# Kernel optimization log

Hardware: AMD Instinct MI355X
Metric: run time of the kernel (lower is better)

## Reference

```python
import jax, jax.numpy as jnp
import numpy as np

B = 16          # frames in batch
N = 16384       # atoms (num_nodes)
R = 1024        # residues (segments)
D = 320         # input_dim
BINS = 32       # adaptive-pool feature bins (output_size_per_segment[1])
H = 512         # mlp_hidden_dim
COND = 3        # conditioner dim (X_ref)
EPS = 1e-5


def setup_inputs() -> dict:
    key = jax.random.key(0)
    ks = jax.random.split(key, 8)
    x = jax.random.normal(ks[0], (B * N, D), dtype=jnp.float32)
    cond = jax.random.normal(ks[1], (N, COND), dtype=jnp.float32)
    # sorted residue ids -> contiguous variable-size segments, like real residues
    seg_ids = jnp.sort(jax.random.randint(ks[2], (N,), 0, R, dtype=jnp.int32))
    W1 = jax.random.normal(ks[3], (BINS + COND, H), dtype=jnp.float32) * 0.05
    b1 = jnp.zeros((H,), jnp.float32)
    gamma = jnp.ones((H,), jnp.float32)
    beta = jnp.zeros((H,), jnp.float32)
    bn_mean = jnp.zeros((H,), jnp.float32)
    bn_var = jnp.ones((H,), jnp.float32)
    W2 = jax.random.normal(ks[4], (H, 3), dtype=jnp.float32) * 0.05
    b2 = jnp.zeros((3,), jnp.float32)
    return {"x": x, "cond": cond, "seg_ids": seg_ids, "W1": W1, "b1": b1,
            "gamma": gamma, "beta": beta, "bn_mean": bn_mean, "bn_var": bn_var,
            "W2": W2, "b2": b2}


def reference(x, cond, seg_ids, W1, b1, gamma, beta, bn_mean, bn_var, W2, b2):
    # x: [B*N, D] atom embeddings
    x3 = x.reshape(B, N, D)
    # --- per-residue AdaptiveAvgPool2d((1, BINS)) as a fused segment mean ---
    # output height 1 == mean over all atoms of the residue
    counts = jax.ops.segment_sum(jnp.ones((N,), x.dtype), seg_ids, num_segments=R)
    sums = jax.vmap(lambda xb: jax.ops.segment_sum(xb, seg_ids, num_segments=R))(x3)  # [B,R,D]
    seg_mean = sums / jnp.maximum(counts, 1.0)[None, :, None]
    # adaptive width D -> BINS (D divisible by BINS => exact chunk means)
    pooled = seg_mean.reshape(B, R, BINS, D // BINS).mean(-1)  # [B,R,BINS]
    # --- broadcast residue feature back to atoms, concat conditioner ---
    per_atom = pooled[:, seg_ids, :]                           # [B,N,BINS]
    cond_b = jnp.broadcast_to(cond[None], (B, N, COND))
    feat = jnp.concatenate([per_atom, cond_b], axis=-1).reshape(B * N, BINS + COND)
    # --- decoder MLP: Linear -> ReLU -> BatchNorm1d(eval) -> Linear ---
    h = jnp.maximum(feat @ W1 + b1, 0.0)
    h = (h - bn_mean) * jax.lax.rsqrt(bn_var + EPS) * gamma + beta
    out = h @ W2 + b2                                          # [B*N, 3]
    return out
```

## Files before the change

kernel.cpp:

```cpp
#include <hip/hip_runtime.h>
#include <math.h>

#define B_ 16
#define N_ 16384
#define R_ 1024
#define D_ 320
#define BINS_ 32
#define H_ 512
#define EPS_ 1e-5f
#define AP 516
#define EP 260

__global__ __launch_bounds__(256) void k_prep(const int* __restrict__ seg,
                      const float* __restrict__ gamma, const float* __restrict__ beta,
                      const float* __restrict__ mean, const float* __restrict__ var,
                      const float* __restrict__ W2, const float* __restrict__ b2,
                      int* __restrict__ off, float* __restrict__ W2f,
                      float* __restrict__ bias3, float* __restrict__ pooled){
  __shared__ float red[3 * 256];
  int blk = blockIdx.x, tid = threadIdx.x;
  if (blk < 5){
    int g = blk * 256 + tid;
    if (g <= R_){
      int lo = 0, hi = N_;
      while (lo < hi){ int mid = (lo + hi) >> 1; if (seg[mid] < g) lo = mid + 1; else hi = mid; }
      off[g] = lo;
    }
  } else if (blk == 5){
    float p0 = 0.f, p1 = 0.f, p2 = 0.f;
    for (int h = tid; h < H_; h += 256){
      float c = gamma[h] / sqrtf(var[h] + EPS_);
      float d = beta[h] - mean[h] * c;
      float w0 = W2[h * 3 + 0], w1 = W2[h * 3 + 1], w2 = W2[h * 3 + 2];
      W2f[h * 3 + 0] = c * w0; W2f[h * 3 + 1] = c * w1; W2f[h * 3 + 2] = c * w2;
      p0 += d * w0; p1 += d * w1; p2 += d * w2;
    }
    red[tid] = p0; red[256 + tid] = p1; red[512 + tid] = p2;
    __syncthreads();
    for (int s = 128; s > 0; s >>= 1){
      if (tid < s){
        red[tid] += red[tid + s];
        red[256 + tid] += red[256 + tid + s];
        red[512 + tid] += red[512 + tid + s];
      }
      __syncthreads();
    }
    if (tid < 3) bias3[tid] = b2[tid] + red[tid * 256];
  } else {
    float4 z = {0.f, 0.f, 0.f, 0.f};
    float4* p4 = (float4*)pooled;
    const int total4 = B_ * R_ * BINS_ / 4;
    for (int i = (blk - 6) * 256 + tid; i < total4; i += 32 * 256) p4[i] = z;
  }
}

__global__ __launch_bounds__(320) void k_pool(const float* __restrict__ x,
                                              const int* __restrict__ seg,
                                              float* __restrict__ pooled){
  __shared__ int sseg[64];
  __shared__ __align__(16) float red2[4 * 320];
  int c = blockIdx.x, b = blockIdx.y, tid = threadIdx.x;
  int base = c * 64;
  if (tid < 64) sseg[tid] = seg[base + tid];
  __syncthreads();
  int rowoff = tid / 80;
  int col4 = tid - rowoff * 80;
  const float4* xp = (const float4*)x + ((size_t)b * N_ + base) * 80 + col4;
  int i = 0;
  while (i < 64){
    int sg = sseg[i];
    int e = i + 1;
    while (e < 64 && sseg[e] == sg) e++;
    float4 acc = {0.f, 0.f, 0.f, 0.f};
    for (int r = i + rowoff; r < e; r += 4){
      float4 v = xp[(size_t)r * 80];
      acc.x += v.x; acc.y += v.y; acc.z += v.z; acc.w += v.w;
    }
    *(float4*)&red2[rowoff * 320 + col4 * 4] = acc;
    __syncthreads();
    if (tid < 32){
      float s = 0.f;
      #pragma unroll
      for (int ro = 0; ro < 4; ro++)
        #pragma unroll
        for (int j = 0; j < 10; j++) s += red2[ro * 320 + tid * 10 + j];
      atomicAdd(&pooled[((size_t)b * R_ + sg) * BINS_ + tid], s);
    }
    __syncthreads();
    i = e;
  }
}

__global__ __launch_bounds__(256) void k_main(const float* __restrict__ pooled, const float* __restrict__ cond,
                      const float* __restrict__ W1, const float* __restrict__ b1,
                      const int* __restrict__ off, const float* __restrict__ W2f,
                      const float* __restrict__ bias3, float* __restrict__ out){
  __shared__ __align__(16) float P[B_ * BINS_];
  __shared__ __align__(16) float A[B_ * AP];
  __shared__ __align__(16) float E[16 * EP];
  __shared__ float condT[16 * 3];
  int tid = threadIdx.x;
  int r = blockIdx.x;
  int s = off[r];
  int cnt = off[r + 1] - s;
  if (cnt == 0) return;

  float sc = 1.0f / (float)(cnt * 10);
  for (int i = tid; i < B_ * BINS_; i += 256)
    P[i] = pooled[(size_t)((i >> 5) * R_ + r) * BINS_ + (i & 31)] * sc;
  __syncthreads();

  for (int h = tid; h < H_; h += 256){
    float bb = b1[h];
    float acc[B_];
    #pragma unroll
    for (int b = 0; b < B_; b++) acc[b] = bb;
    #pragma unroll
    for (int k = 0; k < BINS_; k++){
      float w = W1[k * H_ + h];
      #pragma unroll
      for (int b = 0; b < B_; b++) acc[b] += P[b * BINS_ + k] * w;
    }
    #pragma unroll
    for (int b = 0; b < B_; b++) A[b * AP + h] = acc[b];
  }

  int a = tid >> 4, b = tid & 15;
  for (int t0 = 0; t0 < cnt; t0 += 16){
    int na = min(16, cnt - t0);
    __syncthreads();
    if (tid < 48){
      int aa = tid / 3, cc = tid % 3;
      condT[tid] = (aa < na) ? cond[(size_t)(s + t0 + aa) * 3 + cc] : 0.f;
    }
    __syncthreads();
    float o0 = 0.f, o1 = 0.f, o2 = 0.f;
    int ae = a < na ? a : 0;
    for (int hc = 0; hc < 2; hc++){
      int h = (hc << 8) + tid;
      float w0 = W1[32 * H_ + h], w1 = W1[33 * H_ + h], w2 = W1[34 * H_ + h];
      for (int aa = 0; aa < na; aa++)
        E[aa * EP + tid] = condT[aa * 3] * w0 + condT[aa * 3 + 1] * w1 + condT[aa * 3 + 2] * w2;
      __syncthreads();
      const float* Ap = &A[b * AP + (hc << 8)];
      const float* Ep = &E[ae * EP];
      const float* Wp = &W2f[(hc << 8) * 3];
      #pragma unroll 4
      for (int hp = 0; hp < 256; hp += 4){
        float4 av = *(const float4*)(Ap + hp);
        float4 ev = *(const float4*)(Ep + hp);
        const float* w = Wp + hp * 3;
        float z;
        z = av.x + ev.x; z = fmaxf(z, 0.f); o0 = fmaf(z, w[0], o0); o1 = fmaf(z, w[1], o1); o2 = fmaf(z, w[2], o2);
        z = av.y + ev.y; z = fmaxf(z, 0.f); o0 = fmaf(z, w[3], o0); o1 = fmaf(z, w[4], o1); o2 = fmaf(z, w[5], o2);
        z = av.z + ev.z; z = fmaxf(z, 0.f); o0 = fmaf(z, w[6], o0); o1 = fmaf(z, w[7], o1); o2 = fmaf(z, w[8], o2);
        z = av.w + ev.w; z = fmaxf(z, 0.f); o0 = fmaf(z, w[9], o0); o1 = fmaf(z, w[10], o1); o2 = fmaf(z, w[11], o2);
      }
      __syncthreads();
    }
    if (a < na){
      size_t oi = ((size_t)b * N_ + (size_t)(s + t0 + a)) * 3;
      out[oi + 0] = o0 + bias3[0];
      out[oi + 1] = o1 + bias3[1];
      out[oi + 2] = o2 + bias3[2];
    }
  }
}

extern "C" void kernel_launch(void* const* d_in, const int* in_sizes, int n_in,
                              void* d_out, int out_size, void* d_ws, size_t ws_size,
                              hipStream_t stream) {
  const float* x      = (const float*)d_in[0];
  const float* cond   = (const float*)d_in[1];
  const int*   seg    = (const int*)  d_in[2];
  const float* W1     = (const float*)d_in[3];
  const float* b1     = (const float*)d_in[4];
  const float* gamma  = (const float*)d_in[5];
  const float* beta   = (const float*)d_in[6];
  const float* bnmean = (const float*)d_in[7];
  const float* bnvar  = (const float*)d_in[8];
  const float* W2     = (const float*)d_in[9];
  const float* b2     = (const float*)d_in[10];
  float* out = (float*)d_out;

  char* ws = (char*)d_ws;
  int*   seg_off = (int*)ws;
  float* W2f     = (float*)(ws + 8192);
  float* bias3   = (float*)(ws + 14592);
  float* pooled  = (float*)(ws + 16384);

  k_prep<<<dim3(38), dim3(256), 0, stream>>>(seg, gamma, beta, bnmean, bnvar, W2, b2,
                                             seg_off, W2f, bias3, pooled);
  k_pool<<<dim3(N_ / 64, B_), dim3(320), 0, stream>>>(x, seg, pooled);
  k_main<<<dim3(R_), dim3(256), 0, stream>>>(pooled, cond, W1, b1, seg_off, W2f, bias3, out);
}
```

Before: 638.8 us.

## Make segment pooling wave-local with ballot-based boundaries, no block barriers

The pooling kernel now gives each 64-atom chunk to a single wavefront. Segment boundaries come from a shuffle and ballot, and each lane sums five strided columns across the rows. The per-segment reduction happens in wave-private shared memory, so the two block-wide barriers per segment run are gone. The trade is scalar loads in place of float4 loads, and one wave now serially reads every row of a segment run instead of four threads sharing the rows.

```diff
diff --git a/kernel.cpp b/kernel.cpp
--- a/kernel.cpp
+++ b/kernel.cpp
@@ -54,40 +54,39 @@
   }
 }
 
-__global__ __launch_bounds__(320) void k_pool(const float* __restrict__ x,
+__global__ __launch_bounds__(256) void k_pool(const float* __restrict__ x,
                                               const int* __restrict__ seg,
                                               float* __restrict__ pooled){
-  __shared__ int sseg[64];
-  __shared__ __align__(16) float red2[4 * 320];
-  int c = blockIdx.x, b = blockIdx.y, tid = threadIdx.x;
+  __shared__ __align__(16) float red[4 * 320];
+  int tid = threadIdx.x;
+  int wid = tid >> 6, lane = tid & 63;
+  int c = blockIdx.x * 4 + wid;
+  int b = blockIdx.y;
   int base = c * 64;
-  if (tid < 64) sseg[tid] = seg[base + tid];
-  __syncthreads();
-  int rowoff = tid / 80;
-  int col4 = tid - rowoff * 80;
-  const float4* xp = (const float4*)x + ((size_t)b * N_ + base) * 80 + col4;
-  int i = 0;
-  while (i < 64){
-    int sg = sseg[i];
-    int e = i + 1;
-    while (e < 64 && sseg[e] == sg) e++;
-    float4 acc = {0.f, 0.f, 0.f, 0.f};
-    for (int r = i + rowoff; r < e; r += 4){
-      float4 v = xp[(size_t)r * 80];
-      acc.x += v.x; acc.y += v.y; acc.z += v.z; acc.w += v.w;
+  int my_seg = seg[base + lane];
+  int prev = __shfl_up(my_seg, 1);
+  bool bnd = (lane == 0) || (my_seg != prev);
+  unsigned long long mask = __ballot(bnd);
+  const float* xp = x + ((size_t)b * N_ + base) * D_ + lane;
+  float* wred = &red[wid * 320];
+  while (mask){
+    int i = __builtin_ctzll(mask);
+    mask &= mask - 1;
+    int e = mask ? __builtin_ctzll(mask) : 64;
+    int sg = __shfl(my_seg, i);
+    float a0 = 0.f, a1 = 0.f, a2 = 0.f, a3 = 0.f, a4 = 0.f;
+    const float* rp = xp + (size_t)i * D_;
+    for (int r = i; r < e; r++, rp += D_){
+      a0 += rp[0]; a1 += rp[64]; a2 += rp[128]; a3 += rp[192]; a4 += rp[256];
     }
-    *(float4*)&red2[rowoff * 320 + col4 * 4] = acc;
-    __syncthreads();
-    if (tid < 32){
+    wred[lane] = a0; wred[64 + lane] = a1; wred[128 + lane] = a2;
+    wred[192 + lane] = a3; wred[256 + lane] = a4;
+    if (lane < 32){
       float s = 0.f;
       #pragma unroll
-      for (int ro = 0; ro < 4; ro++)
-        #pragma unroll
-        for (int j = 0; j < 10; j++) s += red2[ro * 320 + tid * 10 + j];
-      atomicAdd(&pooled[((size_t)b * R_ + sg) * BINS_ + tid], s);
+      for (int j = 0; j < 10; j++) s += wred[lane * 10 + j];
+      atomicAdd(&pooled[((size_t)b * R_ + sg) * BINS_ + lane], s);
     }
-    __syncthreads();
-    i = e;
   }
 }
 
@@ -191,6 +190,6 @@
 
   k_prep<<<dim3(38), dim3(256), 0, stream>>>(seg, gamma, beta, bnmean, bnvar, W2, b2,
                                              seg_off, W2f, bias3, pooled);
-  k_pool<<<dim3(N_ / 64, B_), dim3(320), 0, stream>>>(x, seg, pooled);
+  k_pool<<<dim3(N_ / 64 / 4, B_), dim3(256), 0, stream>>>(x, seg, pooled);
   k_main<<<dim3(R_), dim3(256), 0, stream>>>(pooled, cond, W1, b1, seg_off, W2f, bias3, out);
 }
```

Result: no change. 634.0 us (-0.8%).
